# Performance work log

Hardware: AMD Instinct MI355X
Metric: run time of the kernel (lower is better)

## Reference

```python
import jax, jax.numpy as jnp
import numpy as np

NUM_ITERS = 6   # Ci = 0..5 compute steps happen before the Ci>5 break
EMA = 0.1       # centers <- centers + 0.1*(centersIter - centers)


def _normalize(x, eps=1e-12):
    # F.normalize(x, dim=1): divide rows by clamped L2 norm
    n = jnp.linalg.norm(x, axis=1, keepdims=True)
    return x / jnp.maximum(n, eps)


def _cos_sim_rows(a, b, eps=1e-8):
    # F.cosine_similarity(a, b, dim=1)
    num = (a * b).sum(axis=1)
    den = jnp.maximum(jnp.linalg.norm(a, axis=1) * jnp.linalg.norm(b, axis=1), eps)
    return num / den


def _compute(X, Xn, centers, num1, num2):
    # X: [N, C] raw points, Xn: row-normalized X, centers: [2, C]
    Cn = _normalize(centers)
    dists = 0.5 * (1.0 - Xn @ Cn.T)                      # [N, 2] cosine distance
    labels = jnp.argmin(dists, axis=1)                    # [N]
    onehot = jax.nn.one_hot(labels, 2, dtype=dists.dtype)  # [N, 2]
    dTh = dists * onehot
    lf = labels.astype(dists.dtype)
    chgNum = lf.sum() + 1.0
    unchgNum = (1.0 - lf).sum() + 1.0
    chgDistMean = dTh[:, 1].sum() / chgNum
    unchgDistMean = dTh[:, 0].sum() / unchgNum
    # varflag=False branch of the original module
    unchgF = jnp.where(dTh[:, 0] > unchgDistMean * num2, 0.0, 1.0 - lf)
    chgF = jnp.where(dTh[:, 1] > chgDistMean / num1, 0.0, lf)
    c_chg = (X * chgF[:, None]).sum(0) / (chgF.sum() + 1.0)      # [C]
    c_unchg = (X * unchgF[:, None]).sum(0) / (unchgF.sum() + 1.0)
    centersIter = jnp.stack([c_unchg, c_chg], axis=0)            # [2, C]
    return dists, labels, onehot, centersIter


def _per_batch(Fb, centerInit, num1, num2):
    # Fb: [C, N] -> points X: [N, C]
    X = Fb.T
    Xn = _normalize(X)
    centers = centerInit
    dists, labels, onehot, centersIter = _compute(X, Xn, centers, num1, num2)
    cinidist = _cos_sim_rows(centersIter, centers)   # computed at Ci==0, shape [2]
    labelPinit = labels
    for t in range(1, NUM_ITERS):
        centers = centers + EMA * (centersIter - centers)
        dists, labels, onehot, centersIter = _compute(X, Xn, centers, num1, num2)
        if t == 1:
            labelPinit = labels   # labels appended when Ci==1
    # outputs appended at the Ci>5 break come from the last (t=5) compute
    return centersIter, labels, onehot, dists, labelPinit, cinidist


def setup_inputs() -> dict:
    key = jax.random.key(0)
    k1, k2 = jax.random.split(key)
    FeatureT = jax.random.normal(k1, (8, 128, 256, 256), dtype=jnp.float32)
    centerInit = jax.random.normal(k2, (2, 128), dtype=jnp.float32)
    return {"FeatureT": FeatureT, "centerInit": centerInit, "num1": 2, "num2": 2}


def reference(FeatureT, centerInit, num1, num2):
    B = FeatureT.shape[0]
    F3 = FeatureT.reshape(FeatureT.shape[0], FeatureT.shape[1], -1)   # [B, C, N]
    centersIter_b, labelsout, labels_onehotout, dist2centerTori, labelPinit, cini_b = jax.vmap(
        _per_batch, in_axes=(0, None, None, None)
    )(F3, centerInit, num1, num2)
    centersIterout = centersIter_b.sum(axis=0) / B                    # [2, C]
    dmin = dist2centerTori.min(axis=1, keepdims=True)                 # min over N -> [B,1,2]
    dmax = dist2centerTori.max(axis=1, keepdims=True)
    Weight = 1.0 - (dist2centerTori - dmin) / (dmax - dmin + 1e-7)
    # torch overwrites Cinidist every batch iteration -> last batch's value survives
    Cinidist = cini_b[-1].sum() / B
    return (centersIterout, labelsout, labels_onehotout, Weight,
            dist2centerTori, labelPinit, Cinidist)
```

## Files before the change

### kernel.cpp

```cpp
#include <hip/hip_runtime.h>
#include <math.h>

#define BATCH 8
#define CH 128
#define NPTS 65536
#define NBLKA 64
#define APTS 1024
#define NBLKB 32
#define BPTS 2048
#define PB_STRIDE 260

static constexpr size_t WS_CENTERS = 0;
static constexpr size_t WS_CITER   = WS_CENTERS + (size_t)BATCH * 2 * CH * sizeof(float);
static constexpr size_t WS_THRESH  = WS_CITER + (size_t)BATCH * 2 * CH * sizeof(float);
static constexpr size_t WS_CINI    = WS_THRESH + 256;
static constexpr size_t WS_PA      = WS_CINI + 256;
static constexpr size_t WS_PMM     = WS_PA + (size_t)BATCH * NBLKA * 4 * sizeof(double);
static constexpr size_t WS_PB      = WS_PMM + (size_t)BATCH * NBLKA * 4 * sizeof(float);

static constexpr size_t OUT_CITER  = 0;
static constexpr size_t OUT_LABELS = 256;
static constexpr size_t OUT_ONEHOT = OUT_LABELS + (size_t)BATCH * NPTS;
static constexpr size_t OUT_WEIGHT = OUT_ONEHOT + (size_t)BATCH * NPTS * 2;
static constexpr size_t OUT_DISTS  = OUT_WEIGHT + (size_t)BATCH * NPTS * 2;
static constexpr size_t OUT_LABELP = OUT_DISTS + (size_t)BATCH * NPTS * 2;
static constexpr size_t OUT_CINID  = OUT_LABELP + (size_t)BATCH * NPTS;

__global__ void initK(const float* __restrict__ cinit, char* __restrict__ ws) {
    const int t = blockIdx.x * blockDim.x + threadIdx.x;
    if (t < BATCH * 2 * CH) {
        ((float*)(ws + WS_CENTERS))[t] = cinit[t & (2 * CH - 1)];
    }
}

template <int TMODE>
__global__ __launch_bounds__(256) void phaseA_k(const float* __restrict__ X,
                                                char* __restrict__ ws,
                                                float* __restrict__ out) {
    const int b = blockIdx.x / NBLKA;
    const int blk = blockIdx.x % NBLKA;
    const int tid = threadIdx.x;
    const int wid = tid >> 6, lane = tid & 63;

    __shared__ float cn[2][CH];
    __shared__ double redd[3][4];
    __shared__ float redmm[4][4];

    const float* centers = (const float*)(ws + WS_CENTERS) + b * 2 * CH;
    if (wid < 2) {
        float v0 = centers[wid * CH + lane];
        float v1 = centers[wid * CH + lane + 64];
        float ssq = v0 * v0 + v1 * v1;
#pragma unroll
        for (int o = 32; o > 0; o >>= 1) ssq += __shfl_down(ssq, o);
        ssq = __shfl(ssq, 0);
        const float inv = 1.0f / fmaxf(sqrtf(ssq), 1e-12f);
        cn[wid][lane] = v0 * inv;
        cn[wid][lane + 64] = v1 * inv;
    }
    __syncthreads();

    const int n0 = blk * APTS + tid * 4;
    const float* Xb = X + (size_t)b * CH * NPTS + n0;
    float4 a0 = make_float4(0, 0, 0, 0), a1 = a0, aq = a0;
#pragma unroll 4
    for (int c = 0; c < CH; ++c) {
        const float4 x = *(const float4*)(Xb + (size_t)c * NPTS);
        const float w0 = cn[0][c], w1 = cn[1][c];
        a0.x += x.x * w0; a0.y += x.y * w0; a0.z += x.z * w0; a0.w += x.w * w0;
        a1.x += x.x * w1; a1.y += x.y * w1; a1.z += x.z * w1; a1.w += x.w * w1;
        aq.x += x.x * x.x; aq.y += x.y * x.y; aq.z += x.z * x.z; aq.w += x.w * x.w;
    }

    float2* distsb = (float2*)(out + OUT_DISTS) + (size_t)b * NPTS;
    double sLf = 0.0, sD0 = 0.0, sD1 = 0.0;
    float mn0 = 1e30f, mx0 = -1e30f, mn1 = 1e30f, mx1 = -1e30f;

    const float s0a[4] = {a0.x, a0.y, a0.z, a0.w};
    const float s1a[4] = {a1.x, a1.y, a1.z, a1.w};
    const float qa[4]  = {aq.x, aq.y, aq.z, aq.w};
#pragma unroll
    for (int k = 0; k < 4; ++k) {
        const int n = n0 + k;
        const float invn = 1.0f / fmaxf(sqrtf(qa[k]), 1e-12f);
        const float d0 = 0.5f * (1.0f - s0a[k] * invn);
        const float d1 = 0.5f * (1.0f - s1a[k] * invn);
        const int lab = d1 < d0;
        distsb[n] = make_float2(d0, d1);
        sLf += (double)lab;
        sD0 += lab ? 0.0 : (double)d0;
        sD1 += lab ? (double)d1 : 0.0;
        if (TMODE == 1) {
            out[OUT_LABELP + (size_t)b * NPTS + n] = (float)lab;
        }
        if (TMODE == 2) {
            const size_t pn = (size_t)b * NPTS + n;
            out[OUT_LABELS + pn] = (float)lab;
            *(float2*)(out + OUT_ONEHOT + pn * 2) = make_float2(lab ? 0.0f : 1.0f, lab ? 1.0f : 0.0f);
            mn0 = fminf(mn0, d0); mx0 = fmaxf(mx0, d0);
            mn1 = fminf(mn1, d1); mx1 = fmaxf(mx1, d1);
        }
    }

#pragma unroll
    for (int o = 32; o > 0; o >>= 1) {
        sLf += __shfl_down(sLf, o);
        sD0 += __shfl_down(sD0, o);
        sD1 += __shfl_down(sD1, o);
    }
    if (lane == 0) { redd[0][wid] = sLf; redd[1][wid] = sD0; redd[2][wid] = sD1; }
    if (TMODE == 2) {
#pragma unroll
        for (int o = 32; o > 0; o >>= 1) {
            mn0 = fminf(mn0, __shfl_down(mn0, o));
            mx0 = fmaxf(mx0, __shfl_down(mx0, o));
            mn1 = fminf(mn1, __shfl_down(mn1, o));
            mx1 = fmaxf(mx1, __shfl_down(mx1, o));
        }
        if (lane == 0) { redmm[0][wid] = mn0; redmm[1][wid] = mx0; redmm[2][wid] = mn1; redmm[3][wid] = mx1; }
    }
    __syncthreads();
    if (tid == 0) {
        double* pA = (double*)(ws + WS_PA) + (size_t)(b * NBLKA + blk) * 4;
        pA[0] = redd[0][0] + redd[0][1] + redd[0][2] + redd[0][3];
        pA[1] = redd[1][0] + redd[1][1] + redd[1][2] + redd[1][3];
        pA[2] = redd[2][0] + redd[2][1] + redd[2][2] + redd[2][3];
        if (TMODE == 2) {
            float* pMM = (float*)(ws + WS_PMM) + (size_t)(b * NBLKA + blk) * 4;
            pMM[0] = fminf(fminf(redmm[0][0], redmm[0][1]), fminf(redmm[0][2], redmm[0][3]));
            pMM[1] = fmaxf(fmaxf(redmm[1][0], redmm[1][1]), fmaxf(redmm[1][2], redmm[1][3]));
            pMM[2] = fminf(fminf(redmm[2][0], redmm[2][1]), fminf(redmm[2][2], redmm[2][3]));
            pMM[3] = fmaxf(fmaxf(redmm[3][0], redmm[3][1]), fmaxf(redmm[3][2], redmm[3][3]));
        }
    }
}

__global__ __launch_bounds__(64) void reduceA_k(char* __restrict__ ws,
                                                const int* __restrict__ n1p,
                                                const int* __restrict__ n2p) {
    const int b = blockIdx.x, tid = threadIdx.x;
    const double* pA = (const double*)(ws + WS_PA) + (size_t)b * NBLKA * 4;
    double sLf = pA[tid * 4 + 0], sD0 = pA[tid * 4 + 1], sD1 = pA[tid * 4 + 2];
#pragma unroll
    for (int o = 32; o > 0; o >>= 1) {
        sLf += __shfl_down(sLf, o);
        sD0 += __shfl_down(sD0, o);
        sD1 += __shfl_down(sD1, o);
    }
    if (tid == 0) {
        const float fn1 = (float)(*n1p), fn2 = (float)(*n2p);
        const double chgNum = sLf + 1.0;
        const double unchgNum = ((double)NPTS - sLf) + 1.0;
        const float chgMean = (float)(sD1 / chgNum);
        const float unchgMean = (float)(sD0 / unchgNum);
        float* th = (float*)(ws + WS_THRESH) + b * 2;
        th[0] = unchgMean * fn2;
        th[1] = chgMean / fn1;
    }
}

__global__ __launch_bounds__(512) void phaseB_k(const float* __restrict__ X,
                                                char* __restrict__ ws,
                                                const float* __restrict__ out) {
    const int b = blockIdx.x / NBLKB, blk = blockIdx.x % NBLKB;
    const int tid = threadIdx.x, wid = tid >> 6, lane = tid & 63;
    const int base = blk * BPTS;

    __shared__ float flgC[BPTS];
    __shared__ float flgU[BPTS];
    __shared__ double redc[2][8];

    const float* th = (const float*)(ws + WS_THRESH) + b * 2;
    const float unchgT = th[0], chgT = th[1];
    const float2* distsb = (const float2*)(out + OUT_DISTS) + (size_t)b * NPTS + base;

    float cc = 0.f, cu = 0.f;
#pragma unroll
    for (int i = 0; i < BPTS / 512; ++i) {
        const int nl = tid + 512 * i;
        const float2 d = distsb[nl];
        const int lab = d.y < d.x;
        const float fc = (lab && d.y <= chgT) ? 1.f : 0.f;
        const float fu = (!lab && d.x <= unchgT) ? 1.f : 0.f;
        flgC[nl] = fc;
        flgU[nl] = fu;
        cc += fc; cu += fu;
    }
    double dcc = (double)cc, dcu = (double)cu;
#pragma unroll
    for (int o = 32; o > 0; o >>= 1) {
        dcc += __shfl_down(dcc, o);
        dcu += __shfl_down(dcu, o);
    }
    if (lane == 0) { redc[0][wid] = dcu; redc[1][wid] = dcc; }
    __syncthreads();

    double* pB = (double*)(ws + WS_PB) + (size_t)(b * NBLKB + blk) * PB_STRIDE;
    if (tid == 0) {
        double tu = 0, tc = 0;
#pragma unroll
        for (int w = 0; w < 8; ++w) { tu += redc[0][w]; tc += redc[1][w]; }
        pB[2 * CH + 0] = tu;
        pB[2 * CH + 1] = tc;
    }

    const float* Xb = X + (size_t)b * CH * NPTS + base;
    for (int c0 = 0; c0 < CH / 8; ++c0) {
        const int c = wid * (CH / 8) + c0;
        const float* Xc = Xb + (size_t)c * NPTS;
        float aC = 0.f, aU = 0.f;
#pragma unroll
        for (int it = 0; it < BPTS / 256; ++it) {
            const int idx = it * 256 + lane * 4;
            const float4 x = *(const float4*)(Xc + idx);
            const float4 fc = *(const float4*)(&flgC[idx]);
            const float4 fu = *(const float4*)(&flgU[idx]);
            aC += x.x * fc.x + x.y * fc.y + x.z * fc.z + x.w * fc.w;
            aU += x.x * fu.x + x.y * fu.y + x.z * fu.z + x.w * fu.w;
        }
#pragma unroll
        for (int o = 32; o > 0; o >>= 1) {
            aC += __shfl_down(aC, o);
            aU += __shfl_down(aU, o);
        }
        if (lane == 0) {
            pB[0 * CH + c] = (double)aU;
            pB[1 * CH + c] = (double)aC;
        }
    }
}

__global__ __launch_bounds__(256) void reduceB_k(char* __restrict__ ws, const int iter) {
    const int b = blockIdx.x, tid = threadIdx.x;
    const int j = tid >> 7, c = tid & (CH - 1);
    const double* pB = (const double*)(ws + WS_PB) + (size_t)b * NBLKB * PB_STRIDE;
    double s = 0.0;
    for (int blk = 0; blk < NBLKB; ++blk) s += pB[(size_t)blk * PB_STRIDE + j * CH + c];
    __shared__ float cnt[2];
    if (tid < 2) {
        double t = 0.0;
        for (int blk = 0; blk < NBLKB; ++blk) t += pB[(size_t)blk * PB_STRIDE + 2 * CH + tid];
        cnt[tid] = (float)t;
    }
    __syncthreads();
    float* centers = (float*)(ws + WS_CENTERS) + b * 2 * CH;
    float* citer = (float*)(ws + WS_CITER) + b * 2 * CH;
    const float denom = cnt[j] + 1.0f;
    const float ci = (float)s / denom;
    const float old = centers[j * CH + c];
    citer[j * CH + c] = ci;
    if (iter == 0) {
        __shared__ float sd[256], sa[256], sb2[256];
        sd[tid] = ci * old; sa[tid] = ci * ci; sb2[tid] = old * old;
        __syncthreads();
        for (int o = 64; o > 0; o >>= 1) {
            if (c < o) { sd[tid] += sd[tid + o]; sa[tid] += sa[tid + o]; sb2[tid] += sb2[tid + o]; }
            __syncthreads();
        }
        if (c == 0) {
            const float den = fmaxf(sqrtf(sa[tid]) * sqrtf(sb2[tid]), 1e-8f);
            ((float*)(ws + WS_CINI))[b * 2 + j] = sd[tid] / den;
        }
    }
    if (iter < 5) centers[j * CH + c] = old + 0.1f * (ci - old);
}

__global__ __launch_bounds__(256) void weightK(char* __restrict__ ws, float* __restrict__ out) {
    const int b = blockIdx.x / NBLKA, blk = blockIdx.x % NBLKA;
    const int tid = threadIdx.x;
    __shared__ float mm[4];
    if (tid < 64) {
        const float* pMM = (const float*)(ws + WS_PMM) + (size_t)b * NBLKA * 4;
        float mn0 = pMM[tid * 4 + 0], mx0 = pMM[tid * 4 + 1];
        float mn1 = pMM[tid * 4 + 2], mx1 = pMM[tid * 4 + 3];
#pragma unroll
        for (int o = 32; o > 0; o >>= 1) {
            mn0 = fminf(mn0, __shfl_down(mn0, o)); mx0 = fmaxf(mx0, __shfl_down(mx0, o));
            mn1 = fminf(mn1, __shfl_down(mn1, o)); mx1 = fmaxf(mx1, __shfl_down(mx1, o));
        }
        if (tid == 0) { mm[0] = mn0; mm[1] = mx0; mm[2] = mn1; mm[3] = mx1; }
    }
    __syncthreads();
    const float den0 = mm[1] - mm[0] + 1e-7f;
    const float den1 = mm[3] - mm[2] + 1e-7f;
    const int n = blk * APTS + tid * 4;
    const float2* distsb = (const float2*)(out + OUT_DISTS) + (size_t)b * NPTS + n;
    const float4 da = *(const float4*)(distsb);
    const float4 db = *(const float4*)(distsb + 2);
    float4 wa, wb;
    wa.x = 1.0f - (da.x - mm[0]) / den0;
    wa.y = 1.0f - (da.y - mm[2]) / den1;
    wa.z = 1.0f - (da.z - mm[0]) / den0;
    wa.w = 1.0f - (da.w - mm[2]) / den1;
    wb.x = 1.0f - (db.x - mm[0]) / den0;
    wb.y = 1.0f - (db.y - mm[2]) / den1;
    wb.z = 1.0f - (db.z - mm[0]) / den0;
    wb.w = 1.0f - (db.w - mm[2]) / den1;
    float* wout = out + OUT_WEIGHT + ((size_t)b * NPTS + n) * 2;
    *(float4*)wout = wa;
    *(float4*)(wout + 4) = wb;

    if (blockIdx.x == 0) {
        const float* citer = (const float*)(ws + WS_CITER);
        double s = 0.0;
        for (int bb = 0; bb < BATCH; ++bb) s += (double)citer[bb * 2 * CH + tid];
        out[OUT_CITER + tid] = (float)(s / (double)BATCH);
        if (tid == 0) {
            const float* cini = (const float*)(ws + WS_CINI);
            out[OUT_CINID] = (cini[(BATCH - 1) * 2 + 0] + cini[(BATCH - 1) * 2 + 1]) / (float)BATCH;
        }
    }
}

extern "C" void kernel_launch(void* const* d_in, const int* in_sizes, int n_in,
                              void* d_out, int out_size, void* d_ws, size_t ws_size,
                              hipStream_t stream) {
    const float* X = (const float*)d_in[0];
    const float* cinit = (const float*)d_in[1];
    const int* num1 = (const int*)d_in[2];
    const int* num2 = (const int*)d_in[3];
    float* out = (float*)d_out;
    char* ws = (char*)d_ws;

    initK<<<8, 256, 0, stream>>>(cinit, ws);
    for (int t = 0; t < 6; ++t) {
        if (t == 1)      phaseA_k<1><<<BATCH * NBLKA, 256, 0, stream>>>(X, ws, out);
        else if (t == 5) phaseA_k<2><<<BATCH * NBLKA, 256, 0, stream>>>(X, ws, out);
        else             phaseA_k<0><<<BATCH * NBLKA, 256, 0, stream>>>(X, ws, out);
        reduceA_k<<<BATCH, 64, 0, stream>>>(ws, num1, num2);
        phaseB_k<<<BATCH * NBLKB, 512, 0, stream>>>(X, ws, out);
        reduceB_k<<<BATCH, 256, 0, stream>>>(ws, t);
    }
    weightK<<<BATCH * NBLKA, 256, 0, stream>>>(ws, out);
}
```

Before: 576.4 us.

## Fold small reduction kernels into the phase A and phase B kernels

Removes the separate init, reduceA, reduceB and weight kernels. Their work is now redundantly recomputed at the start of each phaseA or phaseB block: the partial-sum reduction, the center EMA update and normalization, and the thresholds. Weights are written inside the final phaseB pass, which drops a separate pass over dists. Centers use ping-pong buffers so a block can read the old centers while block 0 writes the new ones. This cuts the launch count from about 26 to 13 and removes serialized tiny kernels, at the cost of every block rereading the PB partials.

```diff
diff --git a/kernel.cpp b/kernel.cpp
--- a/kernel.cpp
+++ b/kernel.cpp
@@ -11,9 +11,7 @@
 #define PB_STRIDE 260
 
 static constexpr size_t WS_CENTERS = 0;
-static constexpr size_t WS_CITER   = WS_CENTERS + (size_t)BATCH * 2 * CH * sizeof(float);
-static constexpr size_t WS_THRESH  = WS_CITER + (size_t)BATCH * 2 * CH * sizeof(float);
-static constexpr size_t WS_CINI    = WS_THRESH + 256;
+static constexpr size_t WS_CINI    = WS_CENTERS + (size_t)2 * BATCH * 2 * CH * sizeof(float);
 static constexpr size_t WS_PA      = WS_CINI + 256;
 static constexpr size_t WS_PMM     = WS_PA + (size_t)BATCH * NBLKA * 4 * sizeof(double);
 static constexpr size_t WS_PB      = WS_PMM + (size_t)BATCH * NBLKA * 4 * sizeof(float);
@@ -26,15 +24,9 @@
 static constexpr size_t OUT_LABELP = OUT_DISTS + (size_t)BATCH * NPTS * 2;
 static constexpr size_t OUT_CINID  = OUT_LABELP + (size_t)BATCH * NPTS;
 
-__global__ void initK(const float* __restrict__ cinit, char* __restrict__ ws) {
-    const int t = blockIdx.x * blockDim.x + threadIdx.x;
-    if (t < BATCH * 2 * CH) {
-        ((float*)(ws + WS_CENTERS))[t] = cinit[t & (2 * CH - 1)];
-    }
-}
-
-template <int TMODE>
+template <int T>
 __global__ __launch_bounds__(256) void phaseA_k(const float* __restrict__ X,
+                                                const float* __restrict__ cinit,
                                                 char* __restrict__ ws,
                                                 float* __restrict__ out) {
     const int b = blockIdx.x / NBLKA;
@@ -46,17 +38,64 @@
     __shared__ double redd[3][4];
     __shared__ float redmm[4][4];
 
-    const float* centers = (const float*)(ws + WS_CENTERS) + b * 2 * CH;
-    if (wid < 2) {
-        float v0 = centers[wid * CH + lane];
-        float v1 = centers[wid * CH + lane + 64];
-        float ssq = v0 * v0 + v1 * v1;
-#pragma unroll
-        for (int o = 32; o > 0; o >>= 1) ssq += __shfl_down(ssq, o);
-        ssq = __shfl(ssq, 0);
-        const float inv = 1.0f / fmaxf(sqrtf(ssq), 1e-12f);
-        cn[wid][lane] = v0 * inv;
-        cn[wid][lane + 64] = v1 * inv;
+    if constexpr (T == 0) {
+        if (wid < 2) {
+            float v0 = cinit[wid * CH + lane];
+            float v1 = cinit[wid * CH + lane + 64];
+            float ssq = v0 * v0 + v1 * v1;
+#pragma unroll
+            for (int o = 32; o > 0; o >>= 1) ssq += __shfl_down(ssq, o);
+            ssq = __shfl(ssq, 0);
+            const float inv = 1.0f / fmaxf(sqrtf(ssq), 1e-12f);
+            cn[wid][lane] = v0 * inv;
+            cn[wid][lane + 64] = v1 * inv;
+        }
+    } else {
+        __shared__ float cnt_s[2];
+        __shared__ float red4[4];
+        const double* pB = (const double*)(ws + WS_PB) + (size_t)b * NBLKB * PB_STRIDE;
+        if (tid < 64) {
+            const int jj = tid >> 5, kb = tid & 31;
+            double v = pB[(size_t)kb * PB_STRIDE + 2 * CH + jj];
+#pragma unroll
+            for (int o = 16; o > 0; o >>= 1) v += __shfl_down(v, o);
+            if ((tid & 31) == 0) cnt_s[jj] = (float)v;
+        }
+        const int j = tid >> 7, c = tid & (CH - 1);
+        double s = 0.0;
+        for (int kb = 0; kb < NBLKB; ++kb) s += pB[(size_t)kb * PB_STRIDE + j * CH + c];
+        __syncthreads();
+        const float ci = (float)s / (cnt_s[j] + 1.0f);
+        const float old = (T == 1)
+            ? cinit[tid]
+            : ((const float*)(ws + WS_CENTERS))[(size_t)((T - 1) & 1) * BATCH * 2 * CH + b * 2 * CH + tid];
+        const float cnew = old + 0.1f * (ci - old);
+        float ss = cnew * cnew;
+#pragma unroll
+        for (int o = 32; o > 0; o >>= 1) ss += __shfl_down(ss, o);
+        if (lane == 0) red4[wid] = ss;
+        __syncthreads();
+        const float nrm = sqrtf(red4[j * 2] + red4[j * 2 + 1]);
+        cn[j][c] = cnew / fmaxf(nrm, 1e-12f);
+        if constexpr (T == 1) {
+            __shared__ float rsd[4], rsa[4], rsb[4];
+            float sd = ci * old, sa = ci * ci, sb = old * old;
+#pragma unroll
+            for (int o = 32; o > 0; o >>= 1) {
+                sd += __shfl_down(sd, o); sa += __shfl_down(sa, o); sb += __shfl_down(sb, o);
+            }
+            if (lane == 0) { rsd[wid] = sd; rsa[wid] = sa; rsb[wid] = sb; }
+            __syncthreads();
+            if (blk == 0 && tid < 2) {
+                const float nsd = rsd[tid * 2] + rsd[tid * 2 + 1];
+                const float nsa = rsa[tid * 2] + rsa[tid * 2 + 1];
+                const float nsb = rsb[tid * 2] + rsb[tid * 2 + 1];
+                ((float*)(ws + WS_CINI))[b * 2 + tid] = nsd / fmaxf(sqrtf(nsa) * sqrtf(nsb), 1e-8f);
+            }
+        }
+        if (blk == 0) {
+            ((float*)(ws + WS_CENTERS))[(size_t)(T & 1) * BATCH * 2 * CH + b * 2 * CH + tid] = cnew;
+        }
     }
     __syncthreads();
 
@@ -90,10 +129,10 @@
         sLf += (double)lab;
         sD0 += lab ? 0.0 : (double)d0;
         sD1 += lab ? (double)d1 : 0.0;
-        if (TMODE == 1) {
+        if (T == 1) {
             out[OUT_LABELP + (size_t)b * NPTS + n] = (float)lab;
         }
-        if (TMODE == 2) {
+        if (T == 5) {
             const size_t pn = (size_t)b * NPTS + n;
             out[OUT_LABELS + pn] = (float)lab;
             *(float2*)(out + OUT_ONEHOT + pn * 2) = make_float2(lab ? 0.0f : 1.0f, lab ? 1.0f : 0.0f);
@@ -109,7 +148,7 @@
         sD1 += __shfl_down(sD1, o);
     }
     if (lane == 0) { redd[0][wid] = sLf; redd[1][wid] = sD0; redd[2][wid] = sD1; }
-    if (TMODE == 2) {
+    if (T == 5) {
 #pragma unroll
         for (int o = 32; o > 0; o >>= 1) {
             mn0 = fminf(mn0, __shfl_down(mn0, o));
@@ -125,7 +164,7 @@
         pA[0] = redd[0][0] + redd[0][1] + redd[0][2] + redd[0][3];
         pA[1] = redd[1][0] + redd[1][1] + redd[1][2] + redd[1][3];
         pA[2] = redd[2][0] + redd[2][1] + redd[2][2] + redd[2][3];
-        if (TMODE == 2) {
+        if (T == 5) {
             float* pMM = (float*)(ws + WS_PMM) + (size_t)(b * NBLKA + blk) * 4;
             pMM[0] = fminf(fminf(redmm[0][0], redmm[0][1]), fminf(redmm[0][2], redmm[0][3]));
             pMM[1] = fmaxf(fmaxf(redmm[1][0], redmm[1][1]), fmaxf(redmm[1][2], redmm[1][3]));
@@ -135,33 +174,12 @@
     }
 }
 
-__global__ __launch_bounds__(64) void reduceA_k(char* __restrict__ ws,
+template <int T>
+__global__ __launch_bounds__(512) void phaseB_k(const float* __restrict__ X,
+                                                char* __restrict__ ws,
+                                                float* __restrict__ out,
                                                 const int* __restrict__ n1p,
                                                 const int* __restrict__ n2p) {
-    const int b = blockIdx.x, tid = threadIdx.x;
-    const double* pA = (const double*)(ws + WS_PA) + (size_t)b * NBLKA * 4;
-    double sLf = pA[tid * 4 + 0], sD0 = pA[tid * 4 + 1], sD1 = pA[tid * 4 + 2];
-#pragma unroll
-    for (int o = 32; o > 0; o >>= 1) {
-        sLf += __shfl_down(sLf, o);
-        sD0 += __shfl_down(sD0, o);
-        sD1 += __shfl_down(sD1, o);
-    }
-    if (tid == 0) {
-        const float fn1 = (float)(*n1p), fn2 = (float)(*n2p);
-        const double chgNum = sLf + 1.0;
-        const double unchgNum = ((double)NPTS - sLf) + 1.0;
-        const float chgMean = (float)(sD1 / chgNum);
-        const float unchgMean = (float)(sD0 / unchgNum);
-        float* th = (float*)(ws + WS_THRESH) + b * 2;
-        th[0] = unchgMean * fn2;
-        th[1] = chgMean / fn1;
-    }
-}
-
-__global__ __launch_bounds__(512) void phaseB_k(const float* __restrict__ X,
-                                                char* __restrict__ ws,
-                                                const float* __restrict__ out) {
     const int b = blockIdx.x / NBLKB, blk = blockIdx.x % NBLKB;
     const int tid = threadIdx.x, wid = tid >> 6, lane = tid & 63;
     const int base = blk * BPTS;
@@ -169,9 +187,40 @@
     __shared__ float flgC[BPTS];
     __shared__ float flgU[BPTS];
     __shared__ double redc[2][8];
-
-    const float* th = (const float*)(ws + WS_THRESH) + b * 2;
-    const float unchgT = th[0], chgT = th[1];
+    __shared__ float thr_s[2];
+    __shared__ float mm[4];
+
+    if (wid == 0) {
+        const double* pA = (const double*)(ws + WS_PA) + (size_t)b * NBLKA * 4;
+        double sLf = pA[lane * 4 + 0], sD0 = pA[lane * 4 + 1], sD1 = pA[lane * 4 + 2];
+#pragma unroll
+        for (int o = 32; o > 0; o >>= 1) {
+            sLf += __shfl_down(sLf, o);
+            sD0 += __shfl_down(sD0, o);
+            sD1 += __shfl_down(sD1, o);
+        }
+        if (lane == 0) {
+            const float fn1 = (float)(*n1p), fn2 = (float)(*n2p);
+            const double chgNum = sLf + 1.0;
+            const double unchgNum = ((double)NPTS - sLf) + 1.0;
+            thr_s[0] = (float)(sD0 / unchgNum) * fn2;
+            thr_s[1] = (float)(sD1 / chgNum) / fn1;
+        }
+    }
+    if (T == 5 && wid == 1) {
+        const float* pMM = (const float*)(ws + WS_PMM) + (size_t)b * NBLKA * 4;
+        const float4 v = *(const float4*)(pMM + lane * 4);
+        float mn0 = v.x, mx0 = v.y, mn1 = v.z, mx1 = v.w;
+#pragma unroll
+        for (int o = 32; o > 0; o >>= 1) {
+            mn0 = fminf(mn0, __shfl_down(mn0, o)); mx0 = fmaxf(mx0, __shfl_down(mx0, o));
+            mn1 = fminf(mn1, __shfl_down(mn1, o)); mx1 = fmaxf(mx1, __shfl_down(mx1, o));
+        }
+        if (lane == 0) { mm[0] = mn0; mm[1] = mx0; mm[2] = mn1; mm[3] = mx1; }
+    }
+    __syncthreads();
+
+    const float unchgT = thr_s[0], chgT = thr_s[1];
     const float2* distsb = (const float2*)(out + OUT_DISTS) + (size_t)b * NPTS + base;
 
     float cc = 0.f, cu = 0.f;
@@ -185,6 +234,13 @@
         flgC[nl] = fc;
         flgU[nl] = fu;
         cc += fc; cu += fu;
+        if (T == 5) {
+            const float den0 = mm[1] - mm[0] + 1e-7f;
+            const float den1 = mm[3] - mm[2] + 1e-7f;
+            float* wout = out + OUT_WEIGHT + ((size_t)b * NPTS + base + nl) * 2;
+            *(float2*)wout = make_float2(1.0f - (d.x - mm[0]) / den0,
+                                         1.0f - (d.y - mm[2]) / den1);
+        }
     }
     double dcc = (double)cc, dcu = (double)cu;
 #pragma unroll
@@ -230,85 +286,30 @@
     }
 }
 
-__global__ __launch_bounds__(256) void reduceB_k(char* __restrict__ ws, const int iter) {
-    const int b = blockIdx.x, tid = threadIdx.x;
-    const int j = tid >> 7, c = tid & (CH - 1);
-    const double* pB = (const double*)(ws + WS_PB) + (size_t)b * NBLKB * PB_STRIDE;
-    double s = 0.0;
-    for (int blk = 0; blk < NBLKB; ++blk) s += pB[(size_t)blk * PB_STRIDE + j * CH + c];
-    __shared__ float cnt[2];
-    if (tid < 2) {
-        double t = 0.0;
-        for (int blk = 0; blk < NBLKB; ++blk) t += pB[(size_t)blk * PB_STRIDE + 2 * CH + tid];
-        cnt[tid] = (float)t;
-    }
-    __syncthreads();
-    float* centers = (float*)(ws + WS_CENTERS) + b * 2 * CH;
-    float* citer = (float*)(ws + WS_CITER) + b * 2 * CH;
-    const float denom = cnt[j] + 1.0f;
-    const float ci = (float)s / denom;
-    const float old = centers[j * CH + c];
-    citer[j * CH + c] = ci;
-    if (iter == 0) {
-        __shared__ float sd[256], sa[256], sb2[256];
-        sd[tid] = ci * old; sa[tid] = ci * ci; sb2[tid] = old * old;
-        __syncthreads();
-        for (int o = 64; o > 0; o >>= 1) {
-            if (c < o) { sd[tid] += sd[tid + o]; sa[tid] += sa[tid + o]; sb2[tid] += sb2[tid + o]; }
-            __syncthreads();
-        }
-        if (c == 0) {
-            const float den = fmaxf(sqrtf(sa[tid]) * sqrtf(sb2[tid]), 1e-8f);
-            ((float*)(ws + WS_CINI))[b * 2 + j] = sd[tid] / den;
-        }
-    }
-    if (iter < 5) centers[j * CH + c] = old + 0.1f * (ci - old);
-}
-
-__global__ __launch_bounds__(256) void weightK(char* __restrict__ ws, float* __restrict__ out) {
-    const int b = blockIdx.x / NBLKA, blk = blockIdx.x % NBLKA;
+__global__ __launch_bounds__(256) void finalK(char* __restrict__ ws, float* __restrict__ out) {
     const int tid = threadIdx.x;
-    __shared__ float mm[4];
-    if (tid < 64) {
-        const float* pMM = (const float*)(ws + WS_PMM) + (size_t)b * NBLKA * 4;
-        float mn0 = pMM[tid * 4 + 0], mx0 = pMM[tid * 4 + 1];
-        float mn1 = pMM[tid * 4 + 2], mx1 = pMM[tid * 4 + 3];
-#pragma unroll
-        for (int o = 32; o > 0; o >>= 1) {
-            mn0 = fminf(mn0, __shfl_down(mn0, o)); mx0 = fmaxf(mx0, __shfl_down(mx0, o));
-            mn1 = fminf(mn1, __shfl_down(mn1, o)); mx1 = fmaxf(mx1, __shfl_down(mx1, o));
-        }
-        if (tid == 0) { mm[0] = mn0; mm[1] = mx0; mm[2] = mn1; mm[3] = mx1; }
-    }
-    __syncthreads();
-    const float den0 = mm[1] - mm[0] + 1e-7f;
-    const float den1 = mm[3] - mm[2] + 1e-7f;
-    const int n = blk * APTS + tid * 4;
-    const float2* distsb = (const float2*)(out + OUT_DISTS) + (size_t)b * NPTS + n;
-    const float4 da = *(const float4*)(distsb);
-    const float4 db = *(const float4*)(distsb + 2);
-    float4 wa, wb;
-    wa.x = 1.0f - (da.x - mm[0]) / den0;
-    wa.y = 1.0f - (da.y - mm[2]) / den1;
-    wa.z = 1.0f - (da.z - mm[0]) / den0;
-    wa.w = 1.0f - (da.w - mm[2]) / den1;
-    wb.x = 1.0f - (db.x - mm[0]) / den0;
-    wb.y = 1.0f - (db.y - mm[2]) / den1;
-    wb.z = 1.0f - (db.z - mm[0]) / den0;
-    wb.w = 1.0f - (db.w - mm[2]) / den1;
-    float* wout = out + OUT_WEIGHT + ((size_t)b * NPTS + n) * 2;
-    *(float4*)wout = wa;
-    *(float4*)(wout + 4) = wb;
-
-    if (blockIdx.x == 0) {
-        const float* citer = (const float*)(ws + WS_CITER);
+    __shared__ float cnt_s[BATCH][2];
+    const double* pB0 = (const double*)(ws + WS_PB);
+    if (tid < 16) {
+        const int bb = tid >> 1, jj = tid & 1;
+        double v = 0.0;
+        for (int kb = 0; kb < NBLKB; ++kb)
+            v += pB0[(size_t)bb * NBLKB * PB_STRIDE + (size_t)kb * PB_STRIDE + 2 * CH + jj];
+        cnt_s[bb][jj] = (float)v;
+    }
+    __syncthreads();
+    const int j = tid >> 7;
+    double acc = 0.0;
+    for (int bb = 0; bb < BATCH; ++bb) {
         double s = 0.0;
-        for (int bb = 0; bb < BATCH; ++bb) s += (double)citer[bb * 2 * CH + tid];
-        out[OUT_CITER + tid] = (float)(s / (double)BATCH);
-        if (tid == 0) {
-            const float* cini = (const float*)(ws + WS_CINI);
-            out[OUT_CINID] = (cini[(BATCH - 1) * 2 + 0] + cini[(BATCH - 1) * 2 + 1]) / (float)BATCH;
-        }
+        for (int kb = 0; kb < NBLKB; ++kb)
+            s += pB0[(size_t)bb * NBLKB * PB_STRIDE + (size_t)kb * PB_STRIDE + tid];
+        acc += (double)((float)s / (cnt_s[bb][j] + 1.0f));
+    }
+    out[OUT_CITER + tid] = (float)(acc / (double)BATCH);
+    if (tid == 0) {
+        const float* cini = (const float*)(ws + WS_CINI);
+        out[OUT_CINID] = (cini[(BATCH - 1) * 2 + 0] + cini[(BATCH - 1) * 2 + 1]) / (float)BATCH;
     }
 }
 
@@ -322,14 +323,20 @@
     float* out = (float*)d_out;
     char* ws = (char*)d_ws;
 
-    initK<<<8, 256, 0, stream>>>(cinit, ws);
-    for (int t = 0; t < 6; ++t) {
-        if (t == 1)      phaseA_k<1><<<BATCH * NBLKA, 256, 0, stream>>>(X, ws, out);
-        else if (t == 5) phaseA_k<2><<<BATCH * NBLKA, 256, 0, stream>>>(X, ws, out);
-        else             phaseA_k<0><<<BATCH * NBLKA, 256, 0, stream>>>(X, ws, out);
-        reduceA_k<<<BATCH, 64, 0, stream>>>(ws, num1, num2);
-        phaseB_k<<<BATCH * NBLKB, 512, 0, stream>>>(X, ws, out);
-        reduceB_k<<<BATCH, 256, 0, stream>>>(ws, t);
-    }
-    weightK<<<BATCH * NBLKA, 256, 0, stream>>>(ws, out);
+    const dim3 gA(BATCH * NBLKA), bA(256);
+    const dim3 gB(BATCH * NBLKB), bB(512);
+
+    phaseA_k<0><<<gA, bA, 0, stream>>>(X, cinit, ws, out);
+    phaseB_k<0><<<gB, bB, 0, stream>>>(X, ws, out, num1, num2);
+    phaseA_k<1><<<gA, bA, 0, stream>>>(X, cinit, ws, out);
+    phaseB_k<1><<<gB, bB, 0, stream>>>(X, ws, out, num1, num2);
+    phaseA_k<2><<<gA, bA, 0, stream>>>(X, cinit, ws, out);
+    phaseB_k<2><<<gB, bB, 0, stream>>>(X, ws, out, num1, num2);
+    phaseA_k<3><<<gA, bA, 0, stream>>>(X, cinit, ws, out);
+    phaseB_k<3><<<gB, bB, 0, stream>>>(X, ws, out, num1, num2);
+    phaseA_k<4><<<gA, bA, 0, stream>>>(X, cinit, ws, out);
+    phaseB_k<4><<<gB, bB, 0, stream>>>(X, ws, out, num1, num2);
+    phaseA_k<5><<<gA, bA, 0, stream>>>(X, cinit, ws, out);
+    phaseB_k<5><<<gB, bB, 0, stream>>>(X, ws, out, num1, num2);
+    finalK<<<1, 256, 0, stream>>>(ws, out);
 }
```

New measurement: 557.2 us. -3.3%, faster.
